# Kernel tuning notes

Hardware: AMD Instinct MI355X
Metric: run time of the kernel (lower is better)

Reference implementation:

```python
import jax, jax.numpy as jnp
import numpy as np

THETA = 10000.0


def _rope(x, pos, theta):
    # x: [..., S, d_k] with d_k even; pos: [..., S] int positions
    d_k = x.shape[-1]
    inv_freq = 1.0 / (theta ** (jnp.arange(0, d_k, 2, dtype=jnp.float32) / d_k))  # [d_k/2]
    ang = pos[..., None].astype(jnp.float32) * inv_freq  # [..., S, d_k/2]
    cos, sin = jnp.cos(ang), jnp.sin(ang)
    x1 = x[..., 0::2]
    x2 = x[..., 1::2]
    r1 = x1 * cos - x2 * sin
    r2 = x1 * sin + x2 * cos
    # interleave back to [..., S, d_k]
    return jnp.stack([r1, r2], axis=-1).reshape(x.shape)


def setup_inputs() -> dict:
    key = jax.random.key(0)
    ks = jax.random.split(key, 5)
    B, S, D = 2, 2048, 1024
    scale = 0.02
    return {
        "in_features": jax.random.normal(ks[0], (B, S, D), dtype=jnp.float32),
        "q_proj": jax.random.normal(ks[1], (D, D), dtype=jnp.float32) * scale,
        "k_proj": jax.random.normal(ks[2], (D, D), dtype=jnp.float32) * scale,
        "v_proj": jax.random.normal(ks[3], (D, D), dtype=jnp.float32) * scale,
        "o_proj": jax.random.normal(ks[4], (D, D), dtype=jnp.float32) * scale,
    }


def reference(in_features, q_proj, k_proj, v_proj, o_proj):
    B, S, D = in_features.shape
    H = 16
    d_k = D // H
    pos = jnp.arange(S)  # broadcast over batch/heads

    def split_heads(x):  # [B,S,D] -> [B,H,S,d_k]
        return x.reshape(B, S, H, d_k).transpose(0, 2, 1, 3)

    Q = split_heads(in_features @ q_proj.T)
    K = split_heads(in_features @ k_proj.T)
    V = split_heads(in_features @ v_proj.T)

    Q = _rope(Q, pos, THETA)
    K = _rope(K, pos, THETA)

    scores = jnp.einsum("bhqd,bhkd->bhqk", Q, K) / jnp.sqrt(jnp.float32(d_k))
    causal = jnp.tril(jnp.ones((S, S), dtype=bool))
    scores = jnp.where(causal, scores, jnp.finfo(scores.dtype).min)
    attn = jax.nn.softmax(scores, axis=-1)
    out = jnp.einsum("bhqk,bhkd->bhqd", attn, V)  # [B,H,S,d_k]
    out = out.transpose(0, 2, 1, 3).reshape(B, S, D)
    return out @ o_proj.T
```

## Files before the change

kernel.cpp:

```cpp
#include <hip/hip_runtime.h>
#include <hip/hip_bf16.h>
#include <math.h>

#define Bdim 2
#define Sdim 2048
#define Ddim 1024
#define Hdim 16
#define DKdim 64
#define Mrows 4096

typedef __attribute__((ext_vector_type(8))) short bf16x8;
typedef __attribute__((ext_vector_type(4))) short short4v;
typedef __attribute__((ext_vector_type(4))) float f32x4;
typedef __attribute__((ext_vector_type(2))) unsigned int uint2v;

#define LOG2E_DIV8 0.18033688011112042f
#define NLOG2TH_64 0.20762050593046016f

__device__ __forceinline__ short f2bf(float f) {
  unsigned int x = __float_as_uint(f);
  x += 0x7fffu + ((x >> 16) & 1u);
  return (short)(x >> 16);
}

__device__ __forceinline__ float fast_exp2(float x) {
#if __has_builtin(__builtin_amdgcn_exp2f)
  return __builtin_amdgcn_exp2f(x);
#else
  return exp2f(x);
#endif
}

__device__ __forceinline__ unsigned int pack_bf2(float lo, float hi) {
  unsigned int r;
  asm("v_cvt_pk_bf16_f32 %0, %1, %2" : "=v"(r) : "v"(lo), "v"(hi));
  return r;
}

__device__ __forceinline__ void gl2lds16(const void* g, void* l) {
  __builtin_amdgcn_global_load_lds(
      (const __attribute__((address_space(1))) void*)g,
      (__attribute__((address_space(3))) void*)l, 16, 0, 0);
}

__global__ __launch_bounds__(256) void prep_kernel(
    const float* __restrict__ X,  const float* __restrict__ Wq,
    const float* __restrict__ Wk, const float* __restrict__ Wv,
    const float* __restrict__ Wo,
    short* __restrict__ Xb, short* __restrict__ Wqkv, short* __restrict__ Wob,
    float2* __restrict__ RT)
{
  const int bid = blockIdx.x;
  if (bid < 8192) {
    int u = bid * 256 + threadIdx.x;
    const float* src; short* dst; int base;
    if (u < 1048576)      { src = X;  dst = Xb;              base = u; }
    else if (u < 1310720) { src = Wq; dst = Wqkv;            base = u - 1048576; }
    else if (u < 1572864) { src = Wk; dst = Wqkv + 1048576;  base = u - 1310720; }
    else if (u < 1835008) { src = Wv; dst = Wqkv + 2097152;  base = u - 1572864; }
    else                  { src = Wo; dst = Wob;             base = u - 1835008; }
    int i = base * 4;
    float4 v = *(const float4*)(src + i);
    short4v o;
    o.x = f2bf(v.x); o.y = f2bf(v.y); o.z = f2bf(v.z); o.w = f2bf(v.w);
    *(short4v*)(dst + i) = o;
  } else {
    int idx = (bid - 8192) * 256 + threadIdx.x;
    int s = idx >> 5, f = idx & 31;
    float inv = exp2f(-NLOG2TH_64 * (float)(2 * f));
    float ang = (float)s * inv;
    float sn, cs;
    sincosf(ang, &sn, &cs);
    RT[idx] = make_float2(sn, cs);
  }
}

template<int MODE>
__global__ __launch_bounds__(256) void gemm_bt(
    const short* __restrict__ A, const short* __restrict__ Bw,
    float* __restrict__ Cf,
    short* __restrict__ Qout, short* __restrict__ Kout, short* __restrict__ Vout,
    const float2* __restrict__ RT,
    int Ndim, int Kdim)
{
  __shared__ __align__(16) short smem[17408];
  short (*st)[136] = (short(*)[136])smem;
  char* smemb = (char*)smem;

  const int tid  = threadIdx.x;
  const int lane = tid & 63;
  const int wid  = tid >> 6;
  const int wr = wid >> 1, wc = wid & 1;
  const int tile_m = blockIdx.x * 128;
  const int tile_n = blockIdx.y * 128;
  const int lrow = lane & 15;
  const int kgrp = lane >> 4;

  const int r0 = tid >> 2;
  const int sc = (tid & 3) * 8;
  const int lA0 = wid * 1024;
  const int lA1 = 4096  + wid * 1024;
  const int lB0 = 8192  + wid * 1024;
  const int lB1 = 12288 + wid * 1024;
  const short* gA0 = A  + (size_t)(tile_m + r0)      * Kdim + sc;
  const short* gA1 = A  + (size_t)(tile_m + r0 + 64) * Kdim + sc;
  const short* gB0 = Bw + (size_t)(tile_n + r0)      * Kdim + sc;
  const short* gB1 = Bw + (size_t)(tile_n + r0 + 64) * Kdim + sc;

  f32x4 acc[4][4];
#pragma unroll
  for (int i = 0; i < 4; i++)
#pragma unroll
    for (int j = 0; j < 4; j++) acc[i][j] = (f32x4)0.0f;

  gl2lds16(gA0, smemb + lA0);
  gl2lds16(gA1, smemb + lA1);
  gl2lds16(gB0, smemb + lB0);
  gl2lds16(gB1, smemb + lB1);
  __syncthreads();

  int cur = 0;
  for (int k0 = 0; k0 < Kdim; k0 += 32) {
    if (k0 + 32 < Kdim) {
      const int nbo = (cur ^ 1) * 16384;
      gl2lds16(gA0 + k0 + 32, smemb + nbo + lA0);
      gl2lds16(gA1 + k0 + 32, smemb + nbo + lA1);
      gl2lds16(gB0 + k0 + 32, smemb + nbo + lB0);
      gl2lds16(gB1 + k0 + 32, smemb + nbo + lB1);
    }
    const int cb = cur * 8192;
    bf16x8 af[4], bfr[4];
#pragma unroll
    for (int i = 0; i < 4; i++)
      af[i]  = *(const bf16x8*)&smem[cb + (wr*64 + i*16 + lrow)*32 + kgrp*8];
#pragma unroll
    for (int j = 0; j < 4; j++)
      bfr[j] = *(const bf16x8*)&smem[cb + 4096 + (wc*64 + j*16 + lrow)*32 + kgrp*8];
#pragma unroll
    for (int i = 0; i < 4; i++)
#pragma unroll
      for (int j = 0; j < 4; j++)
        acc[i][j] = __builtin_amdgcn_mfma_f32_16x16x32_bf16(af[i], bfr[j], acc[i][j], 0, 0, 0);
    __syncthreads();
    cur ^= 1;
  }

  if (MODE == 0) {
#pragma unroll
    for (int i = 0; i < 4; i++)
#pragma unroll
      for (int j = 0; j < 4; j++)
#pragma unroll
        for (int r = 0; r < 4; r++) {
          int mr = tile_m + wr*64 + i*16 + kgrp*4 + r;
          int nc = tile_n + wc*64 + j*16 + lrow;
          Cf[(size_t)mr * Ndim + nc] = acc[i][j][r];
        }
  } else {
    const int sel = tile_n >> 10;
#pragma unroll
    for (int i = 0; i < 4; i++)
#pragma unroll
      for (int j = 0; j < 4; j++)
#pragma unroll
        for (int r = 0; r < 4; r++) {
          float val   = acc[i][j][r];
          float other = __shfl_xor(val, 1, 64);
          int row = wr*64 + i*16 + kgrp*4 + r;
          int col = wc*64 + j*16 + lrow;
          short bv;
          if (sel == 2) {
            bv = f2bf(val);
          } else {
            int c = col & 63;
            int s = (tile_m + row) & 2047;
            float2 t = RT[(s << 5) + (c >> 1)];
            float rot = ((c & 1) == 0) ? (val * t.y - other * t.x)
                                       : (other * t.x + val * t.y);
            if (sel == 0) rot *= LOG2E_DIV8;
            bv = f2bf(rot);
          }
          st[row][col] = bv;
        }
    __syncthreads();
    if (sel < 2) {
      short* Out = (sel == 0) ? Qout : Kout;
#pragma unroll
      for (int p = 0; p < 8; p++) {
        int row = p*16 + (tid >> 4);
        int col = (tid & 15) * 8;
        bf16x8 v = *(const bf16x8*)&st[row][col];
        int mr = tile_m + row; int b = mr >> 11, s = mr & 2047;
        int nc = tile_n + col; int nn = nc & 1023;
        int h = nn >> 6, c = nn & 63;
        *(bf16x8*)&Out[((size_t)((b*Hdim + h)*Sdim + s))*DKdim + c] = v;
      }
    } else {
#pragma unroll
      for (int p = 0; p < 8; p++) {
        int col = p*16 + (tid >> 4);
        int sl  = (tid & 15) * 8;
        bf16x8 v;
#pragma unroll
        for (int e = 0; e < 8; e++) v[e] = st[sl + e][col];
        int nc = tile_n + col; int nn = nc & 1023;
        int h = nn >> 6, c = nn & 63;
        int m0 = tile_m + sl; int b = m0 >> 11, s0 = m0 & 2047;
        *(bf16x8*)&Vout[((size_t)((b*Hdim + h)*DKdim + c))*Sdim + s0] = v;
      }
    }
  }
}

__global__ __launch_bounds__(256, 2) void attn_kernel(
    const short* __restrict__ Q, const short* __restrict__ K,
    const short* __restrict__ Vt, short* __restrict__ O)
{
  const int bh = blockIdx.y;
  const int qt = (bh & 16) ? (int)blockIdx.x : (15 - (int)blockIdx.x);
  const int bq0 = qt * 128;
  const int tid  = threadIdx.x;
  const int wave = tid >> 6;
  const int lane = tid & 63;
  const int lrow = lane & 15, kgrp = lane >> 4;
  const short* Qb = Q  + (size_t)bh * Sdim * DKdim;
  const short* Kb = K  + (size_t)bh * Sdim * DKdim;
  const short* Vb = Vt + (size_t)bh * DKdim * Sdim;

  __shared__ __align__(16) char Kl[2][16384];
  __shared__ __align__(16) char Vl[2][16384];
  __shared__ __align__(16) char lPb[16384];

  const int q0w   = bq0 + wave*32;
  const int NT_w  = (q0w >> 6) + 1;
  const int NTP   = qt + 1;
  const int swz   = (lrow & 7) << 4;
  const int rowbase = wave*4096 + lrow*128;

  const int ldsoff = wave*4096;

  bf16x8 qf[2][2];
#pragma unroll
  for (int t = 0; t < 2; t++) {
    qf[t][0] = *(const bf16x8*)&Qb[(q0w + t*16 + lrow) * DKdim + kgrp*8];
    qf[t][1] = *(const bf16x8*)&Qb[(q0w + t*16 + lrow) * DKdim + 32 + kgrp*8];
  }

  f32x4 o[2][4];
  float psum[2] = {0.0f, 0.0f};
#pragma unroll
  for (int t = 0; t < 2; t++)
#pragma unroll
    for (int n = 0; n < 4; n++) o[t][n] = (f32x4)0.0f;

#pragma unroll
  for (int q = 0; q < 4; q++) {
    int c = wave*256 + q*64 + lane;
    int krow = c >> 3, kc16 = c & 7;
    gl2lds16((const char*)Kb + (size_t)krow * 128 + ((kc16*16) ^ ((krow & 7) << 4)),
             (char*)Kl[0] + ldsoff + q*1024);
    int vrow = c >> 4, vc16 = c & 15;
    gl2lds16((const char*)Vb + (size_t)vrow * (Sdim*2) + ((vc16*16) ^ ((vrow & 7) << 4)),
             (char*)Vl[0] + ldsoff + q*1024);
  }
  __syncthreads();

  int cur = 0;
  for (int it = 0; it < NTP; ++it) {
    const bool havenext = (it + 1 < NTP);
    if (havenext) {
      const int nkv = (it + 1) << 7;
      char* Kd = (char*)Kl[cur ^ 1] + ldsoff;
      char* Vd = (char*)Vl[cur ^ 1] + ldsoff;
#pragma unroll
      for (int q = 0; q < 4; q++) {
        int c = wave*256 + q*64 + lane;
        int krow = c >> 3, kc16 = c & 7;
        gl2lds16((const char*)Kb + (size_t)(nkv + krow) * 128 + ((kc16*16) ^ ((krow & 7) << 4)),
                 Kd + q*1024);
        int vrow = c >> 4, vc16 = c & 15;
        gl2lds16((const char*)Vb + (size_t)vrow * (Sdim*2) + nkv*2 + ((vc16*16) ^ ((vrow & 7) << 4)),
                 Vd + q*1024);
      }
    }
#pragma unroll
    for (int stt = 0; stt < 2; ++stt) {
      const int j = 2*it + stt;
      if (j < NT_w) {
        const int kv0 = j << 6;
        const char* Kc = Kl[cur] + stt*8192;
        const char* Vc = Vl[cur];
        const int vbo = stt*128;
        f32x4 sacc[2][4];
#pragma unroll
        for (int t = 0; t < 2; t++)
#pragma unroll
          for (int nch = 0; nch < 4; nch++) sacc[t][nch] = (f32x4)0.0f;
        __builtin_amdgcn_s_setprio(1);
#pragma unroll
        for (int nch = 0; nch < 4; nch++) {
          int rb = (nch*16 + lrow)*128;
          bf16x8 kf0 = *(const bf16x8*)(Kc + rb + ((kgrp*16) ^ swz));
          bf16x8 kf1 = *(const bf16x8*)(Kc + rb + ((kgrp*16 + 64) ^ swz));
          sacc[0][nch] = __builtin_amdgcn_mfma_f32_16x16x32_bf16(kf0, qf[0][0], sacc[0][nch], 0, 0, 0);
          sacc[0][nch] = __builtin_amdgcn_mfma_f32_16x16x32_bf16(kf1, qf[0][1], sacc[0][nch], 0, 0, 0);
          sacc[1][nch] = __builtin_amdgcn_mfma_f32_16x16x32_bf16(kf0, qf[1][0], sacc[1][nch], 0, 0, 0);
          sacc[1][nch] = __builtin_amdgcn_mfma_f32_16x16x32_bf16(kf1, qf[1][1], sacc[1][nch], 0, 0, 0);
        }
        __builtin_amdgcn_s_setprio(0);
        const bool diag = (j == NT_w - 1);
#pragma unroll
        for (int t = 0; t < 2; t++) {
          const int q_abs = q0w + t*16 + lrow;
#pragma unroll
          for (int nch = 0; nch < 4; nch++) {
            const int kbase = kv0 + nch*16 + kgrp*4;
            float p[4];
#pragma unroll
            for (int r = 0; r < 4; r++) {
              float e = fast_exp2(sacc[t][nch][r]);
              p[r] = (diag && (kbase + r > q_abs)) ? 0.0f : e;
            }
            psum[t] += (p[0] + p[1]) + (p[2] + p[3]);
            uint2v w;
            w.x = pack_bf2(p[0], p[1]);
            w.y = pack_bf2(p[2], p[3]);
            *(uint2v*)(lPb + rowbase + t*2048 + ((nch*32 + kgrp*8) ^ swz)) = w;
          }
        }
        asm volatile("s_waitcnt lgkmcnt(0)" ::: "memory");
        __builtin_amdgcn_sched_barrier(0);
        bf16x8 pa[2][2];
#pragma unroll
        for (int t = 0; t < 2; t++)
#pragma unroll
          for (int h = 0; h < 2; h++)
            pa[t][h] = *(const bf16x8*)(lPb + rowbase + t*2048 + ((h*64 + kgrp*16) ^ swz));
        __builtin_amdgcn_s_setprio(1);
#pragma unroll
        for (int n = 0; n < 4; n++) {
          int rb = (n*16 + lrow)*256 + vbo;
          bf16x8 vf0 = *(const bf16x8*)(Vc + rb + ((kgrp*16) ^ swz));
          bf16x8 vf1 = *(const bf16x8*)(Vc + rb + ((kgrp*16 + 64) ^ swz));
          o[0][n] = __builtin_amdgcn_mfma_f32_16x16x32_bf16(pa[0][0], vf0, o[0][n], 0, 0, 0);
          o[0][n] = __builtin_amdgcn_mfma_f32_16x16x32_bf16(pa[0][1], vf1, o[0][n], 0, 0, 0);
          o[1][n] = __builtin_amdgcn_mfma_f32_16x16x32_bf16(pa[1][0], vf0, o[1][n], 0, 0, 0);
          o[1][n] = __builtin_amdgcn_mfma_f32_16x16x32_bf16(pa[1][1], vf1, o[1][n], 0, 0, 0);
        }
        __builtin_amdgcn_s_setprio(0);
      }
    }
    __syncthreads();
    cur ^= 1;
  }

  float vt[2];
#pragma unroll
  for (int t = 0; t < 2; t++) {
    float v = psum[t];
    v += __shfl_xor(v, 16, 64);
    v += __shfl_xor(v, 32, 64);
    vt[t] = v;
  }
  const int hh = bh & 15, b = bh >> 4;
#pragma unroll
  for (int t = 0; t < 2; t++)
#pragma unroll
    for (int r = 0; r < 4; r++) {
      float rs = __frcp_rn(__shfl(vt[t], kgrp*4 + r, 64));
      int row = q0w + t*16 + kgrp*4 + r;
#pragma unroll
      for (int n = 0; n < 4; n++) {
        int col = hh*64 + n*16 + lrow;
        O[(size_t)(b*Sdim + row) * Ddim + col] = f2bf(o[t][n][r] * rs);
      }
    }
}

extern "C" void kernel_launch(void* const* d_in, const int* in_sizes, int n_in,
                              void* d_out, int out_size, void* d_ws, size_t ws_size,
                              hipStream_t stream) {
  const float* X  = (const float*)d_in[0];
  const float* Wq = (const float*)d_in[1];
  const float* Wk = (const float*)d_in[2];
  const float* Wv = (const float*)d_in[3];
  const float* Wo = (const float*)d_in[4];
  float* out = (float*)d_out;
  char* ws = (char*)d_ws;

  short* Xb   = (short*)(ws);
  short* Wqkv = (short*)(ws + 8388608);
  short* Wob  = (short*)(ws + 14680064);
  short* Qr   = (short*)(ws + 16777216);
  short* Kr   = (short*)(ws + 25165824);
  short* Vt   = (short*)(ws + 33554432);
  short* Ob   = (short*)(ws + 41943040);
  float2* RT  = (float2*)(ws + 41943040);

  prep_kernel<<<8448, 256, 0, stream>>>(X, Wq, Wk, Wv, Wo, Xb, Wqkv, Wob, RT);

  gemm_bt<1><<<dim3(32, 24), 256, 0, stream>>>(Xb, Wqkv, (float*)nullptr,
                                               Qr, Kr, Vt, RT, 3072, 1024);
  attn_kernel<<<dim3(16, 32), 256, 0, stream>>>(Qr, Kr, Vt, Ob);
  gemm_bt<0><<<dim3(32, 8), 256, 0, stream>>>(Ob, Wob, out,
                                              nullptr, nullptr, nullptr, RT, 1024, 1024);
}
```

Measured before the change: 123.1 us.

## Halve attention query tile to 64 rows per block and double the grid

```diff
diff --git a/kernel.cpp b/kernel.cpp
--- a/kernel.cpp
+++ b/kernel.cpp
@@ -217,8 +217,8 @@
     const short* __restrict__ Vt, short* __restrict__ O)
 {
   const int bh = blockIdx.y;
-  const int qt = (bh & 16) ? (int)blockIdx.x : (15 - (int)blockIdx.x);
-  const int bq0 = qt * 128;
+  const int qt = 31 - (int)blockIdx.x;
+  const int bq0 = qt * 64;
   const int tid  = threadIdx.x;
   const int wave = tid >> 6;
   const int lane = tid & 63;
@@ -229,29 +229,23 @@
 
   __shared__ __align__(16) char Kl[2][16384];
   __shared__ __align__(16) char Vl[2][16384];
-  __shared__ __align__(16) char lPb[16384];
-
-  const int q0w   = bq0 + wave*32;
+  __shared__ __align__(16) char lPb[8192];
+
+  const int q0w   = bq0 + wave*16;
   const int NT_w  = (q0w >> 6) + 1;
-  const int NTP   = qt + 1;
+  const int NTP   = (qt >> 1) + 1;
   const int swz   = (lrow & 7) << 4;
-  const int rowbase = wave*4096 + lrow*128;
+  const int rowbase = wave*2048 + lrow*128;
 
   const int ldsoff = wave*4096;
 
-  bf16x8 qf[2][2];
-#pragma unroll
-  for (int t = 0; t < 2; t++) {
-    qf[t][0] = *(const bf16x8*)&Qb[(q0w + t*16 + lrow) * DKdim + kgrp*8];
-    qf[t][1] = *(const bf16x8*)&Qb[(q0w + t*16 + lrow) * DKdim + 32 + kgrp*8];
-  }
-
-  f32x4 o[2][4];
-  float psum[2] = {0.0f, 0.0f};
-#pragma unroll
-  for (int t = 0; t < 2; t++)
-#pragma unroll
-    for (int n = 0; n < 4; n++) o[t][n] = (f32x4)0.0f;
+  bf16x8 qf0 = *(const bf16x8*)&Qb[(q0w + lrow) * DKdim + kgrp*8];
+  bf16x8 qf1 = *(const bf16x8*)&Qb[(q0w + lrow) * DKdim + 32 + kgrp*8];
+
+  f32x4 o[4];
+  float psum = 0.0f;
+#pragma unroll
+  for (int n = 0; n < 4; n++) o[n] = (f32x4)0.0f;
 
 #pragma unroll
   for (int q = 0; q < 4; q++) {
@@ -291,61 +285,48 @@
         const char* Kc = Kl[cur] + stt*8192;
         const char* Vc = Vl[cur];
         const int vbo = stt*128;
-        f32x4 sacc[2][4];
-#pragma unroll
-        for (int t = 0; t < 2; t++)
-#pragma unroll
-          for (int nch = 0; nch < 4; nch++) sacc[t][nch] = (f32x4)0.0f;
+        f32x4 sacc[4];
+#pragma unroll
+        for (int nch = 0; nch < 4; nch++) sacc[nch] = (f32x4)0.0f;
         __builtin_amdgcn_s_setprio(1);
 #pragma unroll
         for (int nch = 0; nch < 4; nch++) {
           int rb = (nch*16 + lrow)*128;
           bf16x8 kf0 = *(const bf16x8*)(Kc + rb + ((kgrp*16) ^ swz));
           bf16x8 kf1 = *(const bf16x8*)(Kc + rb + ((kgrp*16 + 64) ^ swz));
-          sacc[0][nch] = __builtin_amdgcn_mfma_f32_16x16x32_bf16(kf0, qf[0][0], sacc[0][nch], 0, 0, 0);
-          sacc[0][nch] = __builtin_amdgcn_mfma_f32_16x16x32_bf16(kf1, qf[0][1], sacc[0][nch], 0, 0, 0);
-          sacc[1][nch] = __builtin_amdgcn_mfma_f32_16x16x32_bf16(kf0, qf[1][0], sacc[1][nch], 0, 0, 0);
-          sacc[1][nch] = __builtin_amdgcn_mfma_f32_16x16x32_bf16(kf1, qf[1][1], sacc[1][nch], 0, 0, 0);
+          sacc[nch] = __builtin_amdgcn_mfma_f32_16x16x32_bf16(kf0, qf0, sacc[nch], 0, 0, 0);
+          sacc[nch] = __builtin_amdgcn_mfma_f32_16x16x32_bf16(kf1, qf1, sacc[nch], 0, 0, 0);
         }
         __builtin_amdgcn_s_setprio(0);
         const bool diag = (j == NT_w - 1);
-#pragma unroll
-        for (int t = 0; t < 2; t++) {
-          const int q_abs = q0w + t*16 + lrow;
-#pragma unroll
-          for (int nch = 0; nch < 4; nch++) {
-            const int kbase = kv0 + nch*16 + kgrp*4;
-            float p[4];
-#pragma unroll
-            for (int r = 0; r < 4; r++) {
-              float e = fast_exp2(sacc[t][nch][r]);
-              p[r] = (diag && (kbase + r > q_abs)) ? 0.0f : e;
-            }
-            psum[t] += (p[0] + p[1]) + (p[2] + p[3]);
-            uint2v w;
-            w.x = pack_bf2(p[0], p[1]);
-            w.y = pack_bf2(p[2], p[3]);
-            *(uint2v*)(lPb + rowbase + t*2048 + ((nch*32 + kgrp*8) ^ swz)) = w;
+        const int q_abs = q0w + lrow;
+#pragma unroll
+        for (int nch = 0; nch < 4; nch++) {
+          const int kbase = kv0 + nch*16 + kgrp*4;
+          float p[4];
+#pragma unroll
+          for (int r = 0; r < 4; r++) {
+            float e = fast_exp2(sacc[nch][r]);
+            p[r] = (diag && (kbase + r > q_abs)) ? 0.0f : e;
           }
+          psum += (p[0] + p[1]) + (p[2] + p[3]);
+          uint2v w;
+          w.x = pack_bf2(p[0], p[1]);
+          w.y = pack_bf2(p[2], p[3]);
+          *(uint2v*)(lPb + rowbase + ((nch*32 + kgrp*8) ^ swz)) = w;
         }
         asm volatile("s_waitcnt lgkmcnt(0)" ::: "memory");
         __builtin_amdgcn_sched_barrier(0);
-        bf16x8 pa[2][2];
-#pragma unroll
-        for (int t = 0; t < 2; t++)
-#pragma unroll
-          for (int h = 0; h < 2; h++)
-            pa[t][h] = *(const bf16x8*)(lPb + rowbase + t*2048 + ((h*64 + kgrp*16) ^ swz));
+        bf16x8 pa0 = *(const bf16x8*)(lPb + rowbase + ((kgrp*16) ^ swz));
+        bf16x8 pa1 = *(const bf16x8*)(lPb + rowbase + ((64 + kgrp*16) ^ swz));
         __builtin_amdgcn_s_setprio(1);
 #pragma unroll
         for (int n = 0; n < 4; n++) {
           int rb = (n*16 + lrow)*256 + vbo;
           bf16x8 vf0 = *(const bf16x8*)(Vc + rb + ((kgrp*16) ^ swz));
           bf16x8 vf1 = *(const bf16x8*)(Vc + rb + ((kgrp*16 + 64) ^ swz));
-          o[0][n] = __builtin_amdgcn_mfma_f32_16x16x32_bf16(pa[0][0], vf0, o[0][n], 0, 0, 0);
-          o[0][n] = __builtin_amdgcn_mfma_f32_16x16x32_bf16(pa[0][1], vf1, o[0][n], 0, 0, 0);
-          o[1][n] = __builtin_amdgcn_mfma_f32_16x16x32_bf16(pa[1][0], vf0, o[1][n], 0, 0, 0);
-          o[1][n] = __builtin_amdgcn_mfma_f32_16x16x32_bf16(pa[1][1], vf1, o[1][n], 0, 0, 0);
+          o[n] = __builtin_amdgcn_mfma_f32_16x16x32_bf16(pa0, vf0, o[n], 0, 0, 0);
+          o[n] = __builtin_amdgcn_mfma_f32_16x16x32_bf16(pa1, vf1, o[n], 0, 0, 0);
         }
         __builtin_amdgcn_s_setprio(0);
       }
@@ -354,27 +335,20 @@
     cur ^= 1;
   }
 
-  float vt[2];
-#pragma unroll
-  for (int t = 0; t < 2; t++) {
-    float v = psum[t];
-    v += __shfl_xor(v, 16, 64);
-    v += __shfl_xor(v, 32, 64);
-    vt[t] = v;
-  }
+  float v = psum;
+  v += __shfl_xor(v, 16, 64);
+  v += __shfl_xor(v, 32, 64);
   const int hh = bh & 15, b = bh >> 4;
 #pragma unroll
-  for (int t = 0; t < 2; t++)
-#pragma unroll
-    for (int r = 0; r < 4; r++) {
-      float rs = __frcp_rn(__shfl(vt[t], kgrp*4 + r, 64));
-      int row = q0w + t*16 + kgrp*4 + r;
-#pragma unroll
-      for (int n = 0; n < 4; n++) {
-        int col = hh*64 + n*16 + lrow;
-        O[(size_t)(b*Sdim + row) * Ddim + col] = f2bf(o[t][n][r] * rs);
-      }
-    }
+  for (int r = 0; r < 4; r++) {
+    float rs = __frcp_rn(__shfl(v, kgrp*4 + r, 64));
+    int row = q0w + kgrp*4 + r;
+#pragma unroll
+    for (int n = 0; n < 4; n++) {
+      int col = hh*64 + n*16 + lrow;
+      O[(size_t)(b*Sdim + row) * Ddim + col] = f2bf(o[n][r] * rs);
+    }
+  }
 }
 
 extern "C" void kernel_launch(void* const* d_in, const int* in_sizes, int n_in,
@@ -401,7 +375,7 @@
 
   gemm_bt<1><<<dim3(32, 24), 256, 0, stream>>>(Xb, Wqkv, (float*)nullptr,
                                                Qr, Kr, Vt, RT, 3072, 1024);
-  attn_kernel<<<dim3(16, 32), 256, 0, stream>>>(Qr, Kr, Vt, Ob);
+  attn_kernel<<<dim3(32, 32), 256, 0, stream>>>(Qr, Kr, Vt, Ob);
   gemm_bt<0><<<dim3(32, 8), 256, 0, stream>>>(Ob, Wob, out,
                                               nullptr, nullptr, nullptr, RT, 1024, 1024);
 }
```

New measurement: 146.9 us. 19.3% more time.
